# Optimization experiments

Measured on AMD Instinct MI355X. Metric: run time of the kernel, lower is better.

Reference implementation:

```python
import jax, jax.numpy as jnp
import numpy as np
from jax import lax

EPS = 1e-5
C = 232          # inp == oup
BF = C // 2      # branch_features
GROUPS = 2


def bn(x, g, b, m, v):
    # inference batchnorm over channel axis 1 of NCHW
    scale = g / jnp.sqrt(v + EPS)
    return x * scale[None, :, None, None] + (b - m * scale)[None, :, None, None]


def prelu(x, a):
    return jnp.where(x >= 0, x, a.reshape(()) * x)


def conv1x1(x, w):
    # x: [B,C,H,W], w: [O,C]
    return jnp.einsum('bchw,oc->bohw', x, w)


def dwconv3x3(x, w):
    # depthwise 3x3, stride 1, pad 1; w: [C,1,3,3]
    return lax.conv_general_dilated(
        x, w, window_strides=(1, 1), padding=((1, 1), (1, 1)),
        feature_group_count=x.shape[1],
        dimension_numbers=('NCHW', 'OIHW', 'NCHW'))


def setup_inputs() -> dict:
    key = jax.random.key(0)
    ks = jax.random.split(key, 12)
    B, H, W = 64, 56, 56
    inp = {
        'x': jax.random.normal(ks[0], (B, C, H, W), jnp.float32),
        'w2': jax.random.normal(ks[1], (BF, BF), jnp.float32) * 0.1,
        'bn1_g': jax.random.uniform(ks[2], (BF,), jnp.float32, 0.5, 1.5),
        'bn1_b': jax.random.normal(ks[3], (BF,), jnp.float32) * 0.1,
        'bn1_m': jax.random.normal(ks[4], (BF,), jnp.float32) * 0.1,
        'bn1_v': jax.random.uniform(ks[5], (BF,), jnp.float32, 0.5, 1.5),
        'alpha1': jnp.full((1,), 0.25, jnp.float32),
        'wdw': jax.random.normal(ks[6], (BF, 1, 3, 3), jnp.float32) * 0.1,
        'bn2_g': jax.random.uniform(ks[7], (BF,), jnp.float32, 0.5, 1.5),
        'bn2_b': jax.random.normal(ks[8], (BF,), jnp.float32) * 0.1,
        'bn2_m': jax.random.normal(ks[9], (BF,), jnp.float32) * 0.1,
        'bn2_v': jax.random.uniform(ks[10], (BF,), jnp.float32, 0.5, 1.5),
        'w3': jax.random.normal(ks[11], (BF, BF), jnp.float32) * 0.1,
        'bn3_g': jax.random.uniform(jax.random.fold_in(key, 101), (BF,), jnp.float32, 0.5, 1.5),
        'bn3_b': jax.random.normal(jax.random.fold_in(key, 102), (BF,)) * 0.1,
        'bn3_m': jax.random.normal(jax.random.fold_in(key, 103), (BF,)) * 0.1,
        'bn3_v': jax.random.uniform(jax.random.fold_in(key, 104), (BF,), jnp.float32, 0.5, 1.5),
        'alpha2': jnp.full((1,), 0.25, jnp.float32),
    }
    return inp


def reference(x, w2, bn1_g, bn1_b, bn1_m, bn1_v, alpha1, wdw,
              bn2_g, bn2_b, bn2_m, bn2_v, w3, bn3_g, bn3_b, bn3_m, bn3_v, alpha2):
    # stride == 1 path: split channels in half
    x1, x2 = x[:, :BF], x[:, BF:]
    # branch2: 1x1 conv -> BN -> PReLU -> dw3x3 -> BN -> 1x1 conv -> BN -> PReLU
    h = prelu(bn(conv1x1(x2, w2), bn1_g, bn1_b, bn1_m, bn1_v), alpha1)
    h = bn(dwconv3x3(h, wdw), bn2_g, bn2_b, bn2_m, bn2_v)
    h = prelu(bn(conv1x1(h, w3), bn3_g, bn3_b, bn3_m, bn3_v), alpha2)
    out = jnp.concatenate([x1, h], axis=1)
    # channel shuffle (groups=2): out channel k reads input channel (k%2)*cpg + k//2
    cpg = C // GROUPS
    idx = (jnp.arange(C) % GROUPS) * cpg + jnp.arange(C) // GROUPS
    return out[:, idx]
```

## Files before the change

kernel.cpp:

```cpp
#include <hip/hip_runtime.h>
#include <hip/hip_bf16.h>


#define BATCH 64
#define CTOT  232
#define BFC   116
#define HW    3136
#define WD    56
#define CH2   120
#define EPSV  1e-5f

typedef unsigned short u16;
typedef __attribute__((ext_vector_type(8))) short short8;
typedef __attribute__((ext_vector_type(4))) float float4v;

#define WS_W2P   0
#define WS_W3P   32768
#define WS_WDWT  65536
#define WS_B1P   69888
#define WS_B3P   70400
#define WS_H2    131072

__device__ __forceinline__ u16 f2bf(float f) {
    union { float f; unsigned u; } v; v.f = f;
    unsigned r = v.u + 0x7FFF + ((v.u >> 16) & 1);
    return (u16)(r >> 16);
}
__device__ __forceinline__ float bf2f(u16 u) {
    union { unsigned u; float f; } v; v.u = ((unsigned)u) << 16;
    return v.f;
}

__global__ __launch_bounds__(256) void prep(
    const float* __restrict__ w2, const float* __restrict__ g1, const float* __restrict__ b1,
    const float* __restrict__ m1, const float* __restrict__ v1,
    const float* __restrict__ wdw,
    const float* __restrict__ g2, const float* __restrict__ b2,
    const float* __restrict__ m2, const float* __restrict__ v2,
    const float* __restrict__ w3, const float* __restrict__ g3, const float* __restrict__ b3,
    const float* __restrict__ m3, const float* __restrict__ v3,
    char* __restrict__ ws) {
    u16* w2p = (u16*)(ws + WS_W2P);
    u16* w3p = (u16*)(ws + WS_W3P);
    float* wdwt = (float*)(ws + WS_WDWT);
    float* b1p = (float*)(ws + WS_B1P);
    float* b3p = (float*)(ws + WS_B3P);
    int tid = threadIdx.x;
    int bx = blockIdx.x;
    if (bx < 8) {
        int o = bx * 16 + (tid >> 4);
        int cs = (tid & 15) * 8;
        float sc = (o < BFC) ? g1[o] * rsqrtf(v1[o] + EPSV) : 0.f;
        short8 v;
        for (int j = 0; j < 8; j++) {
            int c = cs + j;
            float val = (o < BFC && c < BFC) ? sc * w2[o * BFC + c] : 0.f;
            ((u16*)&v)[j] = f2bf(val);
        }
        *(short8*)&w2p[o * 128 + cs] = v;
    } else if (bx < 16) {
        int o = (bx - 8) * 16 + (tid >> 4);
        int cs = (tid & 15) * 8;
        float sc = (o < BFC) ? g3[o] * rsqrtf(v3[o] + EPSV) : 0.f;
        short8 v;
        for (int j = 0; j < 8; j++) {
            int c = cs + j;
            float val = 0.f;
            if (o < BFC && c < BFC) {
                float sc2 = g2[c] * rsqrtf(v2[c] + EPSV);
                val = sc * sc2 * w3[o * BFC + c];
            }
            ((u16*)&v)[j] = f2bf(val);
        }
        *(short8*)&w3p[o * 128 + cs] = v;
    } else {
        if (tid < CH2)
            for (int tap = 0; tap < 9; tap++)
                wdwt[tap * CH2 + tid] = (tid < BFC) ? wdw[tid * 9 + tap] : 0.f;
        if (tid < 128) {
            float b1v = 0.f, b3v = 0.f;
            if (tid < BFC) {
                float sc1 = g1[tid] * rsqrtf(v1[tid] + EPSV);
                b1v = b1[tid] - m1[tid] * sc1;
                float sc3 = g3[tid] * rsqrtf(v3[tid] + EPSV);
                float s = 0.f;
                for (int c = 0; c < BFC; c++) {
                    float sc2 = g2[c] * rsqrtf(v2[c] + EPSV);
                    float sh2 = b2[c] - m2[c] * sc2;
                    s += w3[tid * BFC + c] * sh2;
                }
                b3v = (b3[tid] - m3[tid] * sc3) + sc3 * s;
            }
            b1p[tid] = b1v;
            b3p[tid] = b3v;
        }
    }
}

__global__ __launch_bounds__(256, 3) void k1(const float* __restrict__ x,
        const float* __restrict__ al1, char* __restrict__ ws) {
    __shared__ u16 h1s[224 * CH2];
    const u16* w2p = (const u16*)(ws + WS_W2P);
    const float* wdwt = (const float*)(ws + WS_WDWT);
    const float* b1p = (const float*)(ws + WS_B1P);
    u16* h2g = (u16*)(ws + WS_H2);

    int tid = threadIdx.x;
    int lane = tid & 63;
    int w = tid >> 6;
    int l15 = lane & 15, kq = lane >> 4;
    int b = blockIdx.y;
    int r0 = blockIdx.x * 2;
    int p_in0 = r0 * WD - WD;

    const float* x2 = x + ((size_t)b * CTOT + BFC) * HW;
    float a1 = al1[0];

    int mh = w >> 1, nh = w & 1;
    short8 bfr[4][4];
    float biasv[4];
    for (int ni = 0; ni < 4; ni++) {
        int o = (nh * 4 + ni) * 16 + l15;
        for (int kt = 0; kt < 4; kt++)
            bfr[ni][kt] = *(const short8*)&w2p[o * 128 + kt * 32 + kq * 8];
        biasv[ni] = b1p[o];
    }
    for (int mi = 0; mi < 7; mi++) {
        int mt = mh * 7 + mi;
        int p = p_in0 + mt * 16 + l15;
        bool pv = (p >= 0) && (p < HW);
        short8 afr[4];
        for (int kt = 0; kt < 4; kt++) {
            short8 av;
            for (int j = 0; j < 8; j++) {
                int c = kt * 32 + kq * 8 + j;
                float v = 0.f;
                if (pv && c < BFC) v = x2[(size_t)c * HW + p];
                ((u16*)&av)[j] = f2bf(v);
            }
            afr[kt] = av;
        }
        for (int ni = 0; ni < 4; ni++) {
            float4v acc = {0.f, 0.f, 0.f, 0.f};
            for (int kt = 0; kt < 4; kt++)
                acc = __builtin_amdgcn_mfma_f32_16x16x32_bf16(afr[kt], bfr[ni][kt], acc, 0, 0, 0);
            int o = (nh * 4 + ni) * 16 + l15;
            if (o < CH2) {
                int plb = mt * 16 + kq * 4;
                for (int r = 0; r < 4; r++) {
                    int pl = plb + r;
                    int pim = p_in0 + pl;
                    float y = acc[r] + biasv[ni];
                    y = y >= 0.f ? y : a1 * y;
                    h1s[pl * CH2 + o] = (pim >= 0 && pim < HW) ? f2bf(y) : (u16)0;
                }
            }
        }
    }
    __syncthreads();

    for (int u = tid; u < 420; u += 256) {
        int oct = u % 15;
        int pq = u / 15;
        int rr = pq / 14;
        int col0 = (pq % 14) * 4;
        float acc[4][8];
        for (int i = 0; i < 4; i++)
            for (int j = 0; j < 8; j++) acc[i][j] = 0.f;
        for (int dy = 0; dy < 3; dy++) {
            int lr = rr + dy;
            float f[6][8];
            for (int k = 0; k < 6; k++) {
                int ci = col0 - 1 + k;
                if (ci >= 0 && ci < WD) {
                    short8 v = *(const short8*)&h1s[(lr * WD + ci) * CH2 + oct * 8];
                    for (int j = 0; j < 8; j++) f[k][j] = bf2f(((const u16*)&v)[j]);
                } else {
                    for (int j = 0; j < 8; j++) f[k][j] = 0.f;
                }
            }
            for (int dx = 0; dx < 3; dx++) {
                const float* wt = &wdwt[(dy * 3 + dx) * CH2 + oct * 8];
                float4v w0 = *(const float4v*)&wt[0];
                float4v w1 = *(const float4v*)&wt[4];
                float w8[8] = {w0[0], w0[1], w0[2], w0[3], w1[0], w1[1], w1[2], w1[3]};
                for (int i = 0; i < 4; i++)
                    for (int j = 0; j < 8; j++)
                        acc[i][j] += f[i + dx][j] * w8[j];
            }
        }
        int prow = (r0 + rr) * WD + col0;
        u16* dst = h2g + ((size_t)b * HW + prow) * CH2 + oct * 8;
        for (int i = 0; i < 4; i++) {
            short8 ov;
            for (int j = 0; j < 8; j++) ((u16*)&ov)[j] = f2bf(acc[i][j]);
            *(short8*)&dst[(size_t)i * CH2] = ov;
        }
    }
}

__global__ __launch_bounds__(256) void k2(const float* __restrict__ x,
        const float* __restrict__ al2, const char* __restrict__ ws,
        float* __restrict__ out) {
    int tid = threadIdx.x;
    int b = blockIdx.y;
    int bx = blockIdx.x;
    if (bx >= 25) {
        int c0 = (bx - 25) * 15;
        int c1 = c0 + 15 < BFC ? c0 + 15 : BFC;
        for (int c = c0; c < c1; c++) {
            const float4v* src = (const float4v*)(x + ((size_t)b * CTOT + c) * HW);
            float4v* dst = (float4v*)(out + ((size_t)b * CTOT + 2 * c) * HW);
            for (int i = tid; i < HW / 4; i += 256) dst[i] = src[i];
        }
        return;
    }
    const u16* w3p = (const u16*)(ws + WS_W3P);
    const float* b3p = (const float*)(ws + WS_B3P);
    const u16* h2g = (const u16*)(ws + WS_H2);
    int lane = tid & 63, w = tid >> 6;
    int l15 = lane & 15, kq = lane >> 4;
    int p0 = bx * 128;
    float a2 = al2[0];
    short8 bfr[2][4];
    float biasv[2];
    for (int i = 0; i < 2; i++) {
        int o = (2 * w + i) * 16 + l15;
        for (int kt = 0; kt < 4; kt++)
            bfr[i][kt] = *(const short8*)&w3p[o * 128 + kt * 32 + kq * 8];
        biasv[i] = b3p[o];
    }
    const u16* h2b = h2g + (size_t)b * HW * CH2;
    short8 z8 = {0, 0, 0, 0, 0, 0, 0, 0};
    for (int mt = 0; mt < 8; mt++) {
        int p = p0 + mt * 16 + l15;
        bool pv = p < HW;
        const u16* arow = h2b + (size_t)p * CH2;
        short8 afr[4];
        for (int kt = 0; kt < 4; kt++) {
            short8 av = z8;
            if (pv && !(kt == 3 && kq == 3)) av = *(const short8*)&arow[kt * 32 + kq * 8];
            afr[kt] = av;
        }
        for (int i = 0; i < 2; i++) {
            float4v acc = {0.f, 0.f, 0.f, 0.f};
            for (int kt = 0; kt < 4; kt++)
                acc = __builtin_amdgcn_mfma_f32_16x16x32_bf16(afr[kt], bfr[i][kt], acc, 0, 0, 0);
            int o = (2 * w + i) * 16 + l15;
            int pq = p0 + mt * 16 + kq * 4;
            if (o < BFC && pq < HW) {
                float4v ov;
                for (int r = 0; r < 4; r++) {
                    float y = acc[r] + biasv[i];
                    ov[r] = y >= 0.f ? y : a2 * y;
                }
                *(float4v*)&out[((size_t)b * CTOT + 2 * o + 1) * HW + pq] = ov;
            }
        }
    }
}

extern "C" void kernel_launch(void* const* d_in, const int* in_sizes, int n_in,
                              void* d_out, int out_size, void* d_ws, size_t ws_size,
                              hipStream_t stream) {
    const float* x   = (const float*)d_in[0];
    const float* w2  = (const float*)d_in[1];
    const float* g1  = (const float*)d_in[2];
    const float* b1  = (const float*)d_in[3];
    const float* m1  = (const float*)d_in[4];
    const float* v1  = (const float*)d_in[5];
    const float* al1 = (const float*)d_in[6];
    const float* wdw = (const float*)d_in[7];
    const float* g2  = (const float*)d_in[8];
    const float* b2  = (const float*)d_in[9];
    const float* m2  = (const float*)d_in[10];
    const float* v2  = (const float*)d_in[11];
    const float* w3  = (const float*)d_in[12];
    const float* g3  = (const float*)d_in[13];
    const float* b3  = (const float*)d_in[14];
    const float* m3  = (const float*)d_in[15];
    const float* v3  = (const float*)d_in[16];
    const float* al2 = (const float*)d_in[17];
    float* out = (float*)d_out;
    char* ws = (char*)d_ws;

    hipLaunchKernelGGL(prep, dim3(17), dim3(256), 0, stream,
                       w2, g1, b1, m1, v1, wdw, g2, b2, m2, v2, w3, g3, b3, m3, v3, ws);
    hipLaunchKernelGGL(k1, dim3(28, BATCH), dim3(256), 0, stream, x, al1, ws);
    hipLaunchKernelGGL(k2, dim3(33, BATCH), dim3(256), 0, stream, x, al2, ws, out);
}
```

Baseline: 529.1 us.

## Fuse second pointwise conv and passthrough copy into dw kernel, pre-transpose input

Adds a transpose kernel that converts the x2 half to bf16 in pixel-major layout, so the first 1x1 conv reads contiguous vector rows instead of doing strided scalar float loads. The depthwise output now stays in shared memory, and the same block runs the second 1x1 conv, PReLU and the x1 passthrough copy. This drops the bf16 h2 intermediate round trip through global memory and removes one kernel launch. In exchange it adds a bf16 transposed copy of x2 in global memory, plus extra syncs and register pressure in the fused kernel.

New measurement: 621.8 us. 1.18x slower.

```diff
diff --git a/kernel.cpp b/kernel.cpp
--- a/kernel.cpp
+++ b/kernel.cpp
@@ -19,7 +19,7 @@
 #define WS_WDWT  65536
 #define WS_B1P   69888
 #define WS_B3P   70400
-#define WS_H2    131072
+#define WS_XT    131072
 
 __device__ __forceinline__ u16 f2bf(float f) {
     union { float f; unsigned u; } v; v.f = f;
@@ -97,13 +97,93 @@
     }
 }
 
+__global__ __launch_bounds__(256) void t0(const float* __restrict__ x, char* __restrict__ ws) {
+    __shared__ u16 lt[64 * CH2];
+    int tid = threadIdx.x;
+    int b = blockIdx.y;
+    int px0 = blockIdx.x * 64;
+    const float* x2 = x + ((size_t)b * CTOT + BFC) * HW;
+    u16* xt = (u16*)(ws + WS_XT);
+    lt[(tid >> 2) * CH2 + BFC + (tid & 3)] = 0;
+    for (int u = tid; u < 58 * 16; u += 256) {
+        int c2 = u >> 4, i = u & 15;
+        int c = c2 * 2;
+        int p = px0 + i * 4;
+        float4v va = *(const float4v*)&x2[(size_t)c * HW + p];
+        float4v vb = *(const float4v*)&x2[(size_t)(c + 1) * HW + p];
+        #pragma unroll
+        for (int j = 0; j < 4; j++) {
+            unsigned pair = (unsigned)f2bf(va[j]) | ((unsigned)f2bf(vb[j]) << 16);
+            *(unsigned*)&lt[(i * 4 + j) * CH2 + c] = pair;
+        }
+    }
+    __syncthreads();
+    for (int u = tid; u < 64 * 15; u += 256) {
+        int px = u / 15, oct = u % 15;
+        short8 v = *(const short8*)&lt[px * CH2 + oct * 8];
+        *(short8*)&xt[((size_t)b * HW + px0 + px) * CH2 + oct * 8] = v;
+    }
+}
+
+__device__ __forceinline__ void dw_compute(const u16* h1s, const float* __restrict__ wdwt,
+                                           int u, short8 hrow[4]) {
+    int oct = u % 15;
+    int pq = u / 15;
+    int rr = pq / 14;
+    int col0 = (pq % 14) * 4;
+    float acc[4][8];
+    #pragma unroll
+    for (int i = 0; i < 4; i++)
+        #pragma unroll
+        for (int j = 0; j < 8; j++) acc[i][j] = 0.f;
+    #pragma unroll
+    for (int dy = 0; dy < 3; dy++) {
+        int lr = rr + dy;
+        float f[6][8];
+        #pragma unroll
+        for (int k = 0; k < 6; k++) {
+            int ci = col0 - 1 + k;
+            if (ci >= 0 && ci < WD) {
+                short8 v = *(const short8*)&h1s[(lr * WD + ci) * CH2 + oct * 8];
+                #pragma unroll
+                for (int j = 0; j < 8; j++) f[k][j] = bf2f(((const u16*)&v)[j]);
+            } else {
+                #pragma unroll
+                for (int j = 0; j < 8; j++) f[k][j] = 0.f;
+            }
+        }
+        #pragma unroll
+        for (int dx = 0; dx < 3; dx++) {
+            const float* wt = &wdwt[(dy * 3 + dx) * CH2 + oct * 8];
+            float4v w0 = *(const float4v*)&wt[0];
+            float4v w1 = *(const float4v*)&wt[4];
+            float w8[8] = {w0[0], w0[1], w0[2], w0[3], w1[0], w1[1], w1[2], w1[3]};
+            #pragma unroll
+            for (int i = 0; i < 4; i++)
+                #pragma unroll
+                for (int j = 0; j < 8; j++)
+                    acc[i][j] += f[i + dx][j] * w8[j];
+        }
+    }
+    #pragma unroll
+    for (int i = 0; i < 4; i++) {
+        short8 ov;
+        #pragma unroll
+        for (int j = 0; j < 8; j++) ((u16*)&ov)[j] = f2bf(acc[i][j]);
+        hrow[i] = ov;
+    }
+}
+
 __global__ __launch_bounds__(256, 3) void k1(const float* __restrict__ x,
-        const float* __restrict__ al1, char* __restrict__ ws) {
+        const float* __restrict__ al1, const float* __restrict__ al2,
+        char* __restrict__ ws, float* __restrict__ out) {
     __shared__ u16 h1s[224 * CH2];
     const u16* w2p = (const u16*)(ws + WS_W2P);
+    const u16* w3p = (const u16*)(ws + WS_W3P);
     const float* wdwt = (const float*)(ws + WS_WDWT);
     const float* b1p = (const float*)(ws + WS_B1P);
-    u16* h2g = (u16*)(ws + WS_H2);
+    const float* b3p = (const float*)(ws + WS_B3P);
+    const u16* xt = (const u16*)(ws + WS_XT);
 
     int tid = threadIdx.x;
     int lane = tid & 63;
@@ -112,150 +192,132 @@
     int b = blockIdx.y;
     int r0 = blockIdx.x * 2;
     int p_in0 = r0 * WD - WD;
-
-    const float* x2 = x + ((size_t)b * CTOT + BFC) * HW;
+    int p_out0 = r0 * WD;
+
+    const u16* xtb = xt + (size_t)b * HW * CH2;
     float a1 = al1[0];
+    short8 z8 = {0, 0, 0, 0, 0, 0, 0, 0};
 
     int mh = w >> 1, nh = w & 1;
-    short8 bfr[4][4];
-    float biasv[4];
-    for (int ni = 0; ni < 4; ni++) {
-        int o = (nh * 4 + ni) * 16 + l15;
-        for (int kt = 0; kt < 4; kt++)
-            bfr[ni][kt] = *(const short8*)&w2p[o * 128 + kt * 32 + kq * 8];
-        biasv[ni] = b1p[o];
-    }
-    for (int mi = 0; mi < 7; mi++) {
-        int mt = mh * 7 + mi;
-        int p = p_in0 + mt * 16 + l15;
-        bool pv = (p >= 0) && (p < HW);
-        short8 afr[4];
-        for (int kt = 0; kt < 4; kt++) {
-            short8 av;
-            for (int j = 0; j < 8; j++) {
-                int c = kt * 32 + kq * 8 + j;
-                float v = 0.f;
-                if (pv && c < BFC) v = x2[(size_t)c * HW + p];
-                ((u16*)&av)[j] = f2bf(v);
-            }
-            afr[kt] = av;
-        }
+    {
+        short8 bfr[4][4];
+        float biasv[4];
         for (int ni = 0; ni < 4; ni++) {
-            float4v acc = {0.f, 0.f, 0.f, 0.f};
+            int o = (nh * 4 + ni) * 16 + l15;
+            #pragma unroll
             for (int kt = 0; kt < 4; kt++)
-                acc = __builtin_amdgcn_mfma_f32_16x16x32_bf16(afr[kt], bfr[ni][kt], acc, 0, 0, 0);
+                bfr[ni][kt] = *(const short8*)&w2p[o * 128 + kt * 32 + kq * 8];
+            biasv[ni] = b1p[o];
+        }
+        #pragma unroll
+        for (int mi = 0; mi < 7; mi++) {
+            int mt = mh * 7 + mi;
+            int p = p_in0 + mt * 16 + l15;
+            bool pv = (p >= 0) && (p < HW);
+            const u16* arow = xtb + (size_t)p * CH2;
+            short8 afr[4];
+            #pragma unroll
+            for (int kt = 0; kt < 4; kt++) {
+                short8 av = z8;
+                if (pv && !(kt == 3 && kq == 3)) av = *(const short8*)&arow[kt * 32 + kq * 8];
+                afr[kt] = av;
+            }
+            for (int ni = 0; ni < 4; ni++) {
+                float4v acc = {0.f, 0.f, 0.f, 0.f};
+                #pragma unroll
+                for (int kt = 0; kt < 4; kt++)
+                    acc = __builtin_amdgcn_mfma_f32_16x16x32_bf16(afr[kt], bfr[ni][kt], acc, 0, 0, 0);
+                int o = (nh * 4 + ni) * 16 + l15;
+                if (o < CH2) {
+                    int plb = mt * 16 + kq * 4;
+                    #pragma unroll
+                    for (int r = 0; r < 4; r++) {
+                        int pl = plb + r;
+                        int pim = p_in0 + pl;
+                        float y = acc[r] + biasv[ni];
+                        y = y >= 0.f ? y : a1 * y;
+                        h1s[pl * CH2 + o] = (pim >= 0 && pim < HW) ? f2bf(y) : (u16)0;
+                    }
+                }
+            }
+        }
+    }
+    __syncthreads();
+
+    short8 hA[4], hB[4];
+    int uA = tid, uB = tid + 256;
+    bool hasB = uB < 420;
+    dw_compute(h1s, wdwt, uA, hA);
+    if (hasB) dw_compute(h1s, wdwt, uB, hB);
+    __syncthreads();
+
+    {
+        int oct = uA % 15, pq = uA / 15;
+        int pl = (pq / 14) * WD + (pq % 14) * 4;
+        #pragma unroll
+        for (int i = 0; i < 4; i++)
+            *(short8*)&h1s[(pl + i) * CH2 + oct * 8] = hA[i];
+    }
+    if (hasB) {
+        int oct = uB % 15, pq = uB / 15;
+        int pl = (pq / 14) * WD + (pq % 14) * 4;
+        #pragma unroll
+        for (int i = 0; i < 4; i++)
+            *(short8*)&h1s[(pl + i) * CH2 + oct * 8] = hB[i];
+    }
+    __syncthreads();
+
+    {
+        float a2 = al2[0];
+        short8 cfr[4][4];
+        float bias3v[4];
+        for (int ni = 0; ni < 4; ni++) {
             int o = (nh * 4 + ni) * 16 + l15;
-            if (o < CH2) {
-                int plb = mt * 16 + kq * 4;
-                for (int r = 0; r < 4; r++) {
-                    int pl = plb + r;
-                    int pim = p_in0 + pl;
-                    float y = acc[r] + biasv[ni];
-                    y = y >= 0.f ? y : a1 * y;
-                    h1s[pl * CH2 + o] = (pim >= 0 && pim < HW) ? f2bf(y) : (u16)0;
+            #pragma unroll
+            for (int kt = 0; kt < 4; kt++)
+                cfr[ni][kt] = *(const short8*)&w3p[o * 128 + kt * 32 + kq * 8];
+            bias3v[ni] = b3p[o];
+        }
+        #pragma unroll
+        for (int mi = 0; mi < 4; mi++) {
+            int mt = mh * 4 + mi;
+            if (mt < 7) {
+                int pl = mt * 16 + l15;
+                const u16* arow = &h1s[pl * CH2];
+                short8 afr[4];
+                #pragma unroll
+                for (int kt = 0; kt < 4; kt++) {
+                    short8 av = z8;
+                    if (!(kt == 3 && kq == 3)) av = *(const short8*)&arow[kt * 32 + kq * 8];
+                    afr[kt] = av;
                 }
-            }
-        }
-    }
-    __syncthreads();
-
-    for (int u = tid; u < 420; u += 256) {
-        int oct = u % 15;
-        int pq = u / 15;
-        int rr = pq / 14;
-        int col0 = (pq % 14) * 4;
-        float acc[4][8];
-        for (int i = 0; i < 4; i++)
-            for (int j = 0; j < 8; j++) acc[i][j] = 0.f;
-        for (int dy = 0; dy < 3; dy++) {
-            int lr = rr + dy;
-            float f[6][8];
-            for (int k = 0; k < 6; k++) {
-                int ci = col0 - 1 + k;
-                if (ci >= 0 && ci < WD) {
-                    short8 v = *(const short8*)&h1s[(lr * WD + ci) * CH2 + oct * 8];
-                    for (int j = 0; j < 8; j++) f[k][j] = bf2f(((const u16*)&v)[j]);
-                } else {
-                    for (int j = 0; j < 8; j++) f[k][j] = 0.f;
+                for (int ni = 0; ni < 4; ni++) {
+                    float4v acc = {0.f, 0.f, 0.f, 0.f};
+                    #pragma unroll
+                    for (int kt = 0; kt < 4; kt++)
+                        acc = __builtin_amdgcn_mfma_f32_16x16x32_bf16(afr[kt], cfr[ni][kt], acc, 0, 0, 0);
+                    int o = (nh * 4 + ni) * 16 + l15;
+                    int pq = mt * 16 + kq * 4;
+                    if (o < BFC) {
+                        float4v ov;
+                        #pragma unroll
+                        for (int r = 0; r < 4; r++) {
+                            float y = acc[r] + bias3v[ni];
+                            ov[r] = y >= 0.f ? y : a2 * y;
+                        }
+                        *(float4v*)&out[((size_t)b * CTOT + 2 * o + 1) * HW + p_out0 + pq] = ov;
+                    }
                 }
             }
-            for (int dx = 0; dx < 3; dx++) {
-                const float* wt = &wdwt[(dy * 3 + dx) * CH2 + oct * 8];
-                float4v w0 = *(const float4v*)&wt[0];
-                float4v w1 = *(const float4v*)&wt[4];
-                float w8[8] = {w0[0], w0[1], w0[2], w0[3], w1[0], w1[1], w1[2], w1[3]};
-                for (int i = 0; i < 4; i++)
-                    for (int j = 0; j < 8; j++)
-                        acc[i][j] += f[i + dx][j] * w8[j];
-            }
-        }
-        int prow = (r0 + rr) * WD + col0;
-        u16* dst = h2g + ((size_t)b * HW + prow) * CH2 + oct * 8;
-        for (int i = 0; i < 4; i++) {
-            short8 ov;
-            for (int j = 0; j < 8; j++) ((u16*)&ov)[j] = f2bf(acc[i][j]);
-            *(short8*)&dst[(size_t)i * CH2] = ov;
-        }
-    }
-}
-
-__global__ __launch_bounds__(256) void k2(const float* __restrict__ x,
-        const float* __restrict__ al2, const char* __restrict__ ws,
-        float* __restrict__ out) {
-    int tid = threadIdx.x;
-    int b = blockIdx.y;
-    int bx = blockIdx.x;
-    if (bx >= 25) {
-        int c0 = (bx - 25) * 15;
-        int c1 = c0 + 15 < BFC ? c0 + 15 : BFC;
-        for (int c = c0; c < c1; c++) {
-            const float4v* src = (const float4v*)(x + ((size_t)b * CTOT + c) * HW);
-            float4v* dst = (float4v*)(out + ((size_t)b * CTOT + 2 * c) * HW);
-            for (int i = tid; i < HW / 4; i += 256) dst[i] = src[i];
-        }
-        return;
-    }
-    const u16* w3p = (const u16*)(ws + WS_W3P);
-    const float* b3p = (const float*)(ws + WS_B3P);
-    const u16* h2g = (const u16*)(ws + WS_H2);
-    int lane = tid & 63, w = tid >> 6;
-    int l15 = lane & 15, kq = lane >> 4;
-    int p0 = bx * 128;
-    float a2 = al2[0];
-    short8 bfr[2][4];
-    float biasv[2];
-    for (int i = 0; i < 2; i++) {
-        int o = (2 * w + i) * 16 + l15;
-        for (int kt = 0; kt < 4; kt++)
-            bfr[i][kt] = *(const short8*)&w3p[o * 128 + kt * 32 + kq * 8];
-        biasv[i] = b3p[o];
-    }
-    const u16* h2b = h2g + (size_t)b * HW * CH2;
-    short8 z8 = {0, 0, 0, 0, 0, 0, 0, 0};
-    for (int mt = 0; mt < 8; mt++) {
-        int p = p0 + mt * 16 + l15;
-        bool pv = p < HW;
-        const u16* arow = h2b + (size_t)p * CH2;
-        short8 afr[4];
-        for (int kt = 0; kt < 4; kt++) {
-            short8 av = z8;
-            if (pv && !(kt == 3 && kq == 3)) av = *(const short8*)&arow[kt * 32 + kq * 8];
-            afr[kt] = av;
-        }
-        for (int i = 0; i < 2; i++) {
-            float4v acc = {0.f, 0.f, 0.f, 0.f};
-            for (int kt = 0; kt < 4; kt++)
-                acc = __builtin_amdgcn_mfma_f32_16x16x32_bf16(afr[kt], bfr[i][kt], acc, 0, 0, 0);
-            int o = (2 * w + i) * 16 + l15;
-            int pq = p0 + mt * 16 + kq * 4;
-            if (o < BFC && pq < HW) {
-                float4v ov;
-                for (int r = 0; r < 4; r++) {
-                    float y = acc[r] + biasv[i];
-                    ov[r] = y >= 0.f ? y : a2 * y;
-                }
-                *(float4v*)&out[((size_t)b * CTOT + 2 * o + 1) * HW + pq] = ov;
-            }
+        }
+    }
+
+    {
+        const float* x1 = x + (size_t)b * CTOT * HW;
+        for (int u = tid; u < BFC * 28; u += 256) {
+            int c = u / 28, i = u % 28;
+            float4v v = *(const float4v*)&x1[(size_t)c * HW + p_out0 + i * 4];
+            *(float4v*)&out[((size_t)b * CTOT + 2 * c) * HW + p_out0 + i * 4] = v;
         }
     }
 }
@@ -286,6 +348,6 @@
 
     hipLaunchKernelGGL(prep, dim3(17), dim3(256), 0, stream,
                        w2, g1, b1, m1, v1, wdw, g2, b2, m2, v2, w3, g3, b3, m3, v3, ws);
-    hipLaunchKernelGGL(k1, dim3(28, BATCH), dim3(256), 0, stream, x, al1, ws);
-    hipLaunchKernelGGL(k2, dim3(33, BATCH), dim3(256), 0, stream, x, al2, ws, out);
-}
+    hipLaunchKernelGGL(t0, dim3(HW / 64, BATCH), dim3(256), 0, stream, x, ws);
+    hipLaunchKernelGGL(k1, dim3(28, BATCH), dim3(256), 0, stream, x, al1, al2, ws, out);
+}
```
